# Optimization experiments

Measured on AMD Instinct MI355X. Metric: run time of the kernel, lower is better.

The kernel has to match this reference:

```python
import jax, jax.numpy as jnp
import numpy as np

HEADS = 8
EMBED = 64
FEAT_A = 256
FEAT_B = 256


def setup_inputs() -> dict:
    key = jax.random.key(0)
    k1, k2, k3, k4, k5 = jax.random.split(key, 5)
    B, N = 2, 2048
    z_a = jax.random.normal(k1, (B, FEAT_A, N), dtype=jnp.float32)
    z_b = jax.random.normal(k2, (B, FEAT_B, N), dtype=jnp.float32)
    # Conv1d(k=1, bias=False) weights, squeezed: [out_ch, in_ch]
    W_a = jax.random.normal(k3, (HEADS * EMBED, FEAT_A), dtype=jnp.float32) * (1.0 / np.sqrt(FEAT_A))
    W_b = jax.random.normal(k4, (HEADS * EMBED, FEAT_B), dtype=jnp.float32) * (1.0 / np.sqrt(FEAT_B))
    W_c = jax.random.normal(k5, (FEAT_A, HEADS * FEAT_B), dtype=jnp.float32) * (1.0 / np.sqrt(HEADS * FEAT_B))
    return {"z_a": z_a, "z_b": z_b, "W_a": W_a, "W_b": W_b, "W_c": W_c}


def reference(z_a, z_b, W_a, W_b, W_c):
    B, Fa, Na = z_a.shape
    Fb = z_b.shape[1]
    H, E = HEADS, EMBED
    norm = 1.0 / np.sqrt(E)
    # 1x1 conv embeddings -> q, k: [B, H, E, N]
    q = jnp.einsum('of,bfn->bon', W_a, z_a).reshape(B, H, E, Na)
    k = jnp.einsum('of,bfn->bon', W_b, z_b).reshape(B, H, E, -1)
    v = z_b  # [B, Fb, K]
    # coeff_pre_softmax[b,h,q,k] = (q^T k) / sqrt(E)
    pre = jnp.einsum('bheq,bhek->bhqk', q, k) * norm
    coeff = jax.nn.softmax(pre, axis=-1)  # softmax over keys (dim=2 in torch bmm form)
    # l1 loss: mean |pre| over (q,k) per head, averaged over heads
    l1 = jnp.mean(jnp.abs(pre), axis=(1, 2, 3))  # [B]
    # feat[b,h,q,f] = coeff @ v^T
    feat = jnp.einsum('bhqk,bfk->bhqf', coeff, v)
    # combine heads: w[h] = W_c[:, h*Fb:(h+1)*Fb].T  -> [H, Fb, Fa]
    w = W_c.reshape(Fa, H, Fb).transpose(1, 2, 0)
    out = jnp.einsum('bhqf,hfo->bqo', feat, w)  # sum over heads
    return out, l1
```

## Files before the change

### kernel.cpp

```cpp
#include <hip/hip_runtime.h>
#include <hip/hip_bf16.h>


#define B_ 2
#define N_ 2048
#define F_ 256
#define H_ 8
#define E_ 64

typedef __attribute__((ext_vector_type(8))) short bf16x8;
typedef __attribute__((ext_vector_type(4))) float f32x4;

__device__ __forceinline__ unsigned short f2b(float x) {
  __hip_bfloat16 h = __float2bfloat16(x);
  return *reinterpret_cast<unsigned short*>(&h);
}

__device__ __forceinline__ unsigned short f2bt(float x) {
  union { float f; unsigned u; } c; c.f = x;
  return (unsigned short)(c.u >> 16);
}

__device__ __forceinline__ f32x4 mfma16(bf16x8 a, bf16x8 b, f32x4 c) {
  return __builtin_amdgcn_mfma_f32_16x16x32_bf16(a, b, c, 0, 0, 0);
}

__device__ __forceinline__ void async_lds16(const unsigned short* g, unsigned short* l) {
  __builtin_amdgcn_global_load_lds(
      (const __attribute__((address_space(1))) unsigned int*)g,
      (__attribute__((address_space(3))) unsigned int*)l, 16, 0, 0);
}

__global__ __launch_bounds__(256) void prep_kernel(
    const float* __restrict__ W_c, unsigned short* __restrict__ wcb,
    const float* __restrict__ W_a, const float* __restrict__ W_b,
    unsigned short* __restrict__ wab, float* __restrict__ l1acc) {
  int i = blockIdx.x * 256 + threadIdx.x;
  if (i < B_) l1acc[i] = 0.f;
  const int nwc = F_ * H_ * F_ / 4;
  const int nw = 512 * F_ / 4;
  const float* src; unsigned short* dst; int j;
  if (i < nwc) { src = W_c; dst = wcb; j = i; }
  else if (i < nwc + nw) { src = W_a; dst = wab; j = i - nwc; }
  else { j = i - nwc - nw; src = W_b; dst = wab + 512 * F_; }
  float4 v = reinterpret_cast<const float4*>(src)[j];
  unsigned long long pk =
      ((unsigned long long)f2b(v.w) << 48) | ((unsigned long long)f2b(v.z) << 32) |
      ((unsigned long long)f2b(v.y) << 16) | (unsigned long long)f2b(v.x);
  reinterpret_cast<unsigned long long*>(dst)[j] = pk;
}

__global__ __launch_bounds__(256) void fused_tp(
    const float* __restrict__ z_a, const float* __restrict__ z_b,
    const unsigned short* __restrict__ wab, unsigned short* __restrict__ vbf,
    unsigned short* __restrict__ qT, unsigned short* __restrict__ kT) {
  __shared__ unsigned int t32[64][33];
  __shared__ __align__(16) unsigned short As[32][256];

  const int tid = threadIdx.x;
  const int nt = blockIdx.x, oh = blockIdx.y, wz = blockIdx.z;
  const int b = wz & 1, which = wz >> 1;
  const float* src = (which ? z_b : z_a) + (size_t)b * F_ * N_;

  const int n4 = (tid & 7) * 4;
  const int frow = tid >> 3;
  const int n_l = tid & 31;
  const int jb = tid >> 5;

#pragma unroll
  for (int s = 0; s < 4; ++s) {
#pragma unroll
    for (int pass = 0; pass < 2; ++pass) {
      int f_l = pass * 32 + frow;
      float4 v = *reinterpret_cast<const float4*>(
          &src[(size_t)(s * 64 + f_l) * N_ + nt * 32 + n4]);
      unsigned short u0 = f2b(v.x), u1 = f2b(v.y), u2 = f2b(v.z), u3 = f2b(v.w);
      t32[f_l][n4] = u0; t32[f_l][n4 + 1] = u1;
      t32[f_l][n4 + 2] = u2; t32[f_l][n4 + 3] = u3;
      if (which && oh == 0) {
        ushort4 pk = {u0, u1, u2, u3};
        *reinterpret_cast<ushort4*>(
            &vbf[(size_t)(b * F_ + s * 64 + f_l) * 2048 + nt * 32 + n4]) = pk;
      }
    }
    __syncthreads();
    {
      int c = s * 8 + jb;
      int p = c ^ n_l;
      unsigned w0 = t32[jb * 8 + 0][n_l] | (t32[jb * 8 + 1][n_l] << 16);
      unsigned w1 = t32[jb * 8 + 2][n_l] | (t32[jb * 8 + 3][n_l] << 16);
      unsigned w2 = t32[jb * 8 + 4][n_l] | (t32[jb * 8 + 5][n_l] << 16);
      unsigned w3 = t32[jb * 8 + 6][n_l] | (t32[jb * 8 + 7][n_l] << 16);
      uint4 pk = {w0, w1, w2, w3};
      *reinterpret_cast<uint4*>(&As[n_l][p * 8]) = pk;
    }
    __syncthreads();
  }

  const int wid = tid >> 6, lane = tid & 63;
  const int quad = lane >> 4, l16 = lane & 15;
  const unsigned short* wsrc = wab + (size_t)which * 512 * F_;
  unsigned short* dst = (which ? kT : qT) + (size_t)b * N_ * 512;
  const float scale = which ? 1.f : 0.125f;
  const f32x4 zero4 = {0.f, 0.f, 0.f, 0.f};

#pragma unroll
  for (int ot = 0; ot < 4; ++ot) {
    const int o = (oh * 4 + ot) * 64 + wid * 16 + l16;
    const unsigned short* brow = wsrc + (size_t)o * F_ + quad * 8;
    f32x4 acc0 = zero4, acc1 = zero4;
#pragma unroll
    for (int kt = 0; kt < 8; ++kt) {
      bf16x8 bf = *reinterpret_cast<const bf16x8*>(brow + kt * 32);
      const int row0 = l16, row1 = 16 + l16;
      bf16x8 a0 = *reinterpret_cast<const bf16x8*>(
          &As[0][0] + row0 * 256 + ((kt * 4 + quad) ^ row0) * 8);
      bf16x8 a1 = *reinterpret_cast<const bf16x8*>(
          &As[0][0] + row1 * 256 + ((kt * 4 + quad) ^ row1) * 8);
      acc0 = mfma16(a0, bf, acc0);
      acc1 = mfma16(a1, bf, acc1);
    }
#pragma unroll
    for (int r = 0; r < 4; ++r) {
      dst[(size_t)(nt * 32 + quad * 4 + r) * 512 + o] = f2b(acc0[r] * scale);
      dst[(size_t)(nt * 32 + 16 + quad * 4 + r) * 512 + o] = f2b(acc1[r] * scale);
    }
  }
}

__global__ __launch_bounds__(256, 3) void attn_mfma(
    const unsigned short* __restrict__ qT, const unsigned short* __restrict__ kT,
    const unsigned short* __restrict__ vbf, unsigned short* __restrict__ feat,
    float* __restrict__ l1acc) {
  __shared__ __align__(16) unsigned short ks[2][32][64];
  __shared__ __align__(16) unsigned short vs[2][256][32];
  __shared__ __align__(16) unsigned short p_blk[2][64][40];
  __shared__ float lsum_sh[64];
  __shared__ float redblk[256];

  const int tid = threadIdx.x;
  const int wid = tid >> 6, lane = tid & 63;
  const int quad = lane >> 4, l16 = lane & 15;
  const int qt = blockIdx.x, h = blockIdx.y, b = blockIdx.z;

  const int kkey = wid * 8 + (lane >> 3);
  const int kchunk = (lane & 7) ^ ((kkey >> 1) & 7);
  const unsigned short* kgl =
      kT + ((size_t)(b * N_ + kkey) * 512) + h * 64 + kchunk * 8;
  const unsigned short* vgl[4];
#pragma unroll
  for (int j = 0; j < 4; ++j) {
    int f = (wid * 4 + j) * 16 + (lane >> 2);
    int c = (lane & 3) ^ ((f >> 1) & 3);
    vgl[j] = vbf + ((size_t)(b * F_ + f) * 2048) + c * 8;
  }

  const unsigned short* qrow =
      qT + (size_t)(b * N_ + qt * 64 + wid * 16 + l16) * 512 + h * 64 + quad * 8;
  bf16x8 qf0 = *reinterpret_cast<const bf16x8*>(qrow);
  bf16x8 qf1 = *reinterpret_cast<const bf16x8*>(qrow + 32);

  const int koff = ((quad ^ (l16 & 7)) * 8);
  const int voff = ((quad ^ ((l16 >> 1) & 3)) * 8);

  f32x4 acc[4][4];
  const f32x4 zero4 = {0.f, 0.f, 0.f, 0.f};
#pragma unroll
  for (int g = 0; g < 4; ++g)
#pragma unroll
    for (int t = 0; t < 4; ++t) acc[g][t] = zero4;
  float lsum[4] = {0.f, 0.f, 0.f, 0.f};
  float suml1 = 0.f;
  bf16x8 vreg[4];

  async_lds16(kgl, &ks[0][wid * 8][0]);
#pragma unroll
  for (int j = 0; j < 4; ++j) async_lds16(vgl[j], &vs[0][(wid * 4 + j) * 16][0]);
  __syncthreads();

#pragma unroll 2
  for (int kt = 0; kt < N_ / 32; ++kt) {
    const int cur = kt & 1;
    if (kt + 1 < N_ / 32) {
      async_lds16(kgl + (size_t)(kt + 1) * 32 * 512, &ks[cur ^ 1][wid * 8][0]);
#pragma unroll
      for (int j = 0; j < 4; ++j)
        async_lds16(vgl[j] + (kt + 1) * 32, &vs[cur ^ 1][(wid * 4 + j) * 16][0]);
    }

    const unsigned short* ksc = &ks[cur][0][0];
    bf16x8 kf00 = *reinterpret_cast<const bf16x8*>(ksc + (2 * l16) * 64 + koff);
    bf16x8 kf01 = *reinterpret_cast<const bf16x8*>(ksc + (2 * l16) * 64 + (koff ^ 32));
    bf16x8 kf10 = *reinterpret_cast<const bf16x8*>(ksc + (2 * l16 + 1) * 64 + koff);
    bf16x8 kf11 = *reinterpret_cast<const bf16x8*>(ksc + (2 * l16 + 1) * 64 + (koff ^ 32));

    f32x4 s0 = mfma16(qf0, kf00, zero4); s0 = mfma16(qf1, kf01, s0);
    f32x4 s1 = mfma16(qf0, kf10, zero4); s1 = mfma16(qf1, kf11, s1);

#pragma unroll
    for (int r = 0; r < 4; ++r) {
      float a0 = s0[r], a1 = s1[r];
      suml1 += fabsf(a0) + fabsf(a1);
      float p0 = __expf(a0), p1 = __expf(a1);
      lsum[r] += p0 + p1;
      unsigned pk = ((unsigned)f2bt(p1) << 16) | f2bt(p0);
      *reinterpret_cast<unsigned*>(&p_blk[cur][wid * 16 + quad * 4 + r][2 * l16]) = pk;
    }

    if (kt > 0) {
#pragma unroll
      for (int g = 0; g < 4; ++g) {
        bf16x8 pf = *reinterpret_cast<const bf16x8*>(&p_blk[cur ^ 1][g * 16 + l16][quad * 8]);
#pragma unroll
        for (int t = 0; t < 4; ++t) acc[g][t] = mfma16(pf, vreg[t], acc[g][t]);
      }
    }

    {
      const unsigned short* vsc = &vs[cur][0][0];
#pragma unroll
      for (int t = 0; t < 4; ++t) {
        int f = wid * 64 + t * 16 + l16;
        vreg[t] = *reinterpret_cast<const bf16x8*>(vsc + f * 32 + voff);
      }
    }
    __syncthreads();
  }

  {
#pragma unroll
    for (int g = 0; g < 4; ++g) {
      bf16x8 pf = *reinterpret_cast<const bf16x8*>(&p_blk[1][g * 16 + l16][quad * 8]);
#pragma unroll
      for (int t = 0; t < 4; ++t) acc[g][t] = mfma16(pf, vreg[t], acc[g][t]);
    }
  }

#pragma unroll
  for (int r = 0; r < 4; ++r) {
    float rs = lsum[r];
    rs += __shfl_xor(rs, 1);
    rs += __shfl_xor(rs, 2);
    rs += __shfl_xor(rs, 4);
    rs += __shfl_xor(rs, 8);
    if (l16 == 0) lsum_sh[wid * 16 + quad * 4 + r] = rs;
  }
  __syncthreads();

#pragma unroll
  for (int g = 0; g < 4; ++g)
#pragma unroll
    for (int r = 0; r < 4; ++r) {
      float invl = 1.f / lsum_sh[g * 16 + quad * 4 + r];
      unsigned short* fr =
          feat + (size_t)(b * N_ + qt * 64 + g * 16 + quad * 4 + r) * 2048 +
          h * 256 + wid * 64 + l16;
#pragma unroll
      for (int t = 0; t < 4; ++t) fr[t * 16] = f2b(acc[g][t][r] * invl);
    }

  redblk[tid] = suml1;
  __syncthreads();
  for (int st = 128; st > 0; st >>= 1) {
    if (tid < st) redblk[tid] += redblk[tid + st];
    __syncthreads();
  }
  if (tid == 0) atomicAdd(&l1acc[b], redblk[0]);
}

__global__ __launch_bounds__(256) void combine_mfma(
    const unsigned short* __restrict__ feat, const unsigned short* __restrict__ wcb,
    const float* __restrict__ l1acc, float* __restrict__ out) {
  __shared__ __align__(16) unsigned short As[2][32][256];

  const int tid = threadIdx.x;
  const int wid = tid >> 6, lane = tid & 63;
  const int quad = lane >> 4, l16 = lane & 15;
  const int mb = blockIdx.x, ob = blockIdx.y;

  const int srow_hi = lane >> 5;
  const int spos = lane & 31;

  const unsigned short* brow = wcb + (size_t)(ob * 64 + wid * 16 + l16) * 2048 + quad * 8;

  f32x4 acc[2];
  const f32x4 zero4 = {0.f, 0.f, 0.f, 0.f};
  acc[0] = zero4; acc[1] = zero4;

#pragma unroll
  for (int i = 0; i < 4; ++i) {
    int row = wid * 8 + 2 * i + srow_hi;
    int cg = spos ^ row;
    async_lds16(feat + (size_t)(mb * 32 + row) * 2048 + cg * 8,
                &As[0][wid * 8 + 2 * i][0]);
  }
  __syncthreads();

  for (int ch = 0; ch < 8; ++ch) {
    const int cur = ch & 1;
    if (ch + 1 < 8) {
#pragma unroll
      for (int i = 0; i < 4; ++i) {
        int row = wid * 8 + 2 * i + srow_hi;
        int cg = spos ^ row;
        async_lds16(feat + (size_t)(mb * 32 + row) * 2048 + (ch + 1) * 256 + cg * 8,
                    &As[cur ^ 1][wid * 8 + 2 * i][0]);
      }
    }
#pragma unroll
    for (int kt = 0; kt < 8; ++kt) {
      bf16x8 bf = *reinterpret_cast<const bf16x8*>(brow + ch * 256 + kt * 32);
#pragma unroll
      for (int g = 0; g < 2; ++g) {
        int row = g * 16 + l16;
        int p = (kt * 4 + quad) ^ row;
        bf16x8 af = *reinterpret_cast<const bf16x8*>(&As[cur][0][0] + row * 256 + p * 8);
        acc[g] = mfma16(af, bf, acc[g]);
      }
    }
    __syncthreads();
  }

#pragma unroll
  for (int g = 0; g < 2; ++g)
#pragma unroll
    for (int r = 0; r < 4; ++r)
      out[(size_t)(mb * 32 + g * 16 + quad * 4 + r) * 256 + ob * 64 + wid * 16 + l16] =
          acc[g][r];

  if (mb == 0 && ob == 0 && tid < B_)
    out[(size_t)B_ * N_ * F_ + tid] = l1acc[tid] * (1.f / (float)(H_ * N_ * N_));
}

extern "C" void kernel_launch(void* const* d_in, const int* in_sizes, int n_in,
                              void* d_out, int out_size, void* d_ws, size_t ws_size,
                              hipStream_t stream) {
  const float* z_a = (const float*)d_in[0];
  const float* z_b = (const float*)d_in[1];
  const float* W_a = (const float*)d_in[2];
  const float* W_b = (const float*)d_in[3];
  const float* W_c = (const float*)d_in[4];
  float* out = (float*)d_out;

  char* ws = (char*)d_ws;
  unsigned short* qT = (unsigned short*)ws;
  unsigned short* kT = (unsigned short*)(ws + ((size_t)4 << 20));
  unsigned short* vbf = (unsigned short*)(ws + ((size_t)8 << 20));
  unsigned short* wcb = (unsigned short*)(ws + ((size_t)10 << 20));
  unsigned short* wab = (unsigned short*)(ws + ((size_t)15 << 20));
  float* l1acc = (float*)(ws + ((size_t)15 << 20) + (768 << 10));
  unsigned short* feat = (unsigned short*)(ws + ((size_t)16 << 20));

  const int nprep = F_ * H_ * F_ / 4 + 2 * (512 * F_ / 4);
  prep_kernel<<<dim3(nprep / 256), 256, 0, stream>>>(
      W_c, wcb, W_a, W_b, wab, l1acc);
  fused_tp<<<dim3(N_ / 32, 2, 4), 256, 0, stream>>>(z_a, z_b, wab, vbf, qT, kT);
  attn_mfma<<<dim3(N_ / 64, H_, B_), 256, 0, stream>>>(qT, kT, vbf, feat, l1acc);
  combine_mfma<<<dim3(B_ * N_ / 32, 4), 256, 0, stream>>>(feat, wcb, l1acc, out);
}
```

Baseline: 163.1 us.

## Keep softmax probabilities in registers via cross-lane shuffles instead of LDS

Computes the score tile transposed (K as the A operand) so that each wave's probabilities can be rearranged into the PV MFMA B-operand with lane shuffles. This removes the shared-memory p_blk round trip and the one-iteration software pipelining of the PV product. Each wave now owns 16 query rows across all 256 features instead of 64 rows by 64 features, which enables vectorized ushort4 stores and a shuffle-only row-sum reduction. The cost is more V fragment loads from LDS per wave (16 per step instead of 4) and 8 shuffles per iteration.

```diff
diff --git a/kernel.cpp b/kernel.cpp
--- a/kernel.cpp
+++ b/kernel.cpp
@@ -134,8 +134,6 @@
     float* __restrict__ l1acc) {
   __shared__ __align__(16) unsigned short ks[2][32][64];
   __shared__ __align__(16) unsigned short vs[2][256][32];
-  __shared__ __align__(16) unsigned short p_blk[2][64][40];
-  __shared__ float lsum_sh[64];
   __shared__ float redblk[256];
 
   const int tid = threadIdx.x;
@@ -160,23 +158,24 @@
   bf16x8 qf0 = *reinterpret_cast<const bf16x8*>(qrow);
   bf16x8 qf1 = *reinterpret_cast<const bf16x8*>(qrow + 32);
 
-  const int koff = ((quad ^ (l16 & 7)) * 8);
+  const int koff2 = ((quad ^ ((l16 >> 1) & 7)) * 8);
   const int voff = ((quad ^ ((l16 >> 1) & 3)) * 8);
 
-  f32x4 acc[4][4];
+  f32x4 acc[16];
   const f32x4 zero4 = {0.f, 0.f, 0.f, 0.f};
 #pragma unroll
-  for (int g = 0; g < 4; ++g)
-#pragma unroll
-    for (int t = 0; t < 4; ++t) acc[g][t] = zero4;
-  float lsum[4] = {0.f, 0.f, 0.f, 0.f};
+  for (int ft = 0; ft < 16; ++ft) acc[ft] = zero4;
+  float lsum_p = 0.f;
   float suml1 = 0.f;
-  bf16x8 vreg[4];
 
   async_lds16(kgl, &ks[0][wid * 8][0]);
 #pragma unroll
   for (int j = 0; j < 4; ++j) async_lds16(vgl[j], &vs[0][(wid * 4 + j) * 16][0]);
   __syncthreads();
+
+  const int srcLo = l16 + ((quad & 1) << 5);
+  const int srcHi = srcLo + 16;
+  const bool hiB = (quad >= 2);
 
 #pragma unroll 2
   for (int kt = 0; kt < N_ / 32; ++kt) {
@@ -189,75 +188,69 @@
     }
 
     const unsigned short* ksc = &ks[cur][0][0];
-    bf16x8 kf00 = *reinterpret_cast<const bf16x8*>(ksc + (2 * l16) * 64 + koff);
-    bf16x8 kf01 = *reinterpret_cast<const bf16x8*>(ksc + (2 * l16) * 64 + (koff ^ 32));
-    bf16x8 kf10 = *reinterpret_cast<const bf16x8*>(ksc + (2 * l16 + 1) * 64 + koff);
-    bf16x8 kf11 = *reinterpret_cast<const bf16x8*>(ksc + (2 * l16 + 1) * 64 + (koff ^ 32));
-
-    f32x4 s0 = mfma16(qf0, kf00, zero4); s0 = mfma16(qf1, kf01, s0);
-    f32x4 s1 = mfma16(qf0, kf10, zero4); s1 = mfma16(qf1, kf11, s1);
-
+    bf16x8 ka0 = *reinterpret_cast<const bf16x8*>(ksc + l16 * 64 + koff2);
+    bf16x8 ka1 = *reinterpret_cast<const bf16x8*>(ksc + l16 * 64 + (koff2 ^ 32));
+    bf16x8 kb0 = *reinterpret_cast<const bf16x8*>(ksc + (16 + l16) * 64 + koff2);
+    bf16x8 kb1 = *reinterpret_cast<const bf16x8*>(ksc + (16 + l16) * 64 + (koff2 ^ 32));
+
+    f32x4 d1 = mfma16(ka0, qf0, zero4); d1 = mfma16(ka1, qf1, d1);
+    f32x4 d2 = mfma16(kb0, qf0, zero4); d2 = mfma16(kb1, qf1, d2);
+
+    float p1[4], p2[4];
 #pragma unroll
     for (int r = 0; r < 4; ++r) {
-      float a0 = s0[r], a1 = s1[r];
+      float a0 = d1[r], a1 = d2[r];
       suml1 += fabsf(a0) + fabsf(a1);
-      float p0 = __expf(a0), p1 = __expf(a1);
-      lsum[r] += p0 + p1;
-      unsigned pk = ((unsigned)f2bt(p1) << 16) | f2bt(p0);
-      *reinterpret_cast<unsigned*>(&p_blk[cur][wid * 16 + quad * 4 + r][2 * l16]) = pk;
-    }
-
-    if (kt > 0) {
-#pragma unroll
-      for (int g = 0; g < 4; ++g) {
-        bf16x8 pf = *reinterpret_cast<const bf16x8*>(&p_blk[cur ^ 1][g * 16 + l16][quad * 8]);
-#pragma unroll
-        for (int t = 0; t < 4; ++t) acc[g][t] = mfma16(pf, vreg[t], acc[g][t]);
-      }
-    }
-
-    {
-      const unsigned short* vsc = &vs[cur][0][0];
-#pragma unroll
-      for (int t = 0; t < 4; ++t) {
-        int f = wid * 64 + t * 16 + l16;
-        vreg[t] = *reinterpret_cast<const bf16x8*>(vsc + f * 32 + voff);
-      }
-    }
-    __syncthreads();
-  }
+      p1[r] = __expf(a0); p2[r] = __expf(a1);
+      lsum_p += p1[r] + p2[r];
+    }
+    unsigned a01 = (unsigned)f2bt(p1[0]) | ((unsigned)f2bt(p1[1]) << 16);
+    unsigned a23 = (unsigned)f2bt(p1[2]) | ((unsigned)f2bt(p1[3]) << 16);
+    unsigned b01 = (unsigned)f2bt(p2[0]) | ((unsigned)f2bt(p2[1]) << 16);
+    unsigned b23 = (unsigned)f2bt(p2[2]) | ((unsigned)f2bt(p2[3]) << 16);
+
+    unsigned sa0 = (unsigned)__shfl((int)a01, srcLo);
+    unsigned sa1 = (unsigned)__shfl((int)a23, srcLo);
+    unsigned sa2 = (unsigned)__shfl((int)a01, srcHi);
+    unsigned sa3 = (unsigned)__shfl((int)a23, srcHi);
+    unsigned sb0 = (unsigned)__shfl((int)b01, srcLo);
+    unsigned sb1 = (unsigned)__shfl((int)b23, srcLo);
+    unsigned sb2 = (unsigned)__shfl((int)b01, srcHi);
+    unsigned sb3 = (unsigned)__shfl((int)b23, srcHi);
+    union { unsigned u[4]; bf16x8 v; } pu;
+    pu.u[0] = hiB ? sb0 : sa0;
+    pu.u[1] = hiB ? sb1 : sa1;
+    pu.u[2] = hiB ? sb2 : sa2;
+    pu.u[3] = hiB ? sb3 : sa3;
+    bf16x8 pfrag = pu.v;
+
+    const unsigned short* vsc = &vs[cur][0][0];
+#pragma unroll
+    for (int ft = 0; ft < 16; ++ft) {
+      bf16x8 vf = *reinterpret_cast<const bf16x8*>(
+          vsc + (ft * 16 + l16) * 32 + voff);
+      acc[ft] = mfma16(vf, pfrag, acc[ft]);
+    }
+
+    __syncthreads();
+  }
+
+  float rs = lsum_p;
+  rs += __shfl_xor(rs, 16);
+  rs += __shfl_xor(rs, 32);
+  float invl = 1.f / rs;
 
   {
-#pragma unroll
-    for (int g = 0; g < 4; ++g) {
-      bf16x8 pf = *reinterpret_cast<const bf16x8*>(&p_blk[1][g * 16 + l16][quad * 8]);
-#pragma unroll
-      for (int t = 0; t < 4; ++t) acc[g][t] = mfma16(pf, vreg[t], acc[g][t]);
-    }
-  }
-
-#pragma unroll
-  for (int r = 0; r < 4; ++r) {
-    float rs = lsum[r];
-    rs += __shfl_xor(rs, 1);
-    rs += __shfl_xor(rs, 2);
-    rs += __shfl_xor(rs, 4);
-    rs += __shfl_xor(rs, 8);
-    if (l16 == 0) lsum_sh[wid * 16 + quad * 4 + r] = rs;
-  }
-  __syncthreads();
-
-#pragma unroll
-  for (int g = 0; g < 4; ++g)
-#pragma unroll
-    for (int r = 0; r < 4; ++r) {
-      float invl = 1.f / lsum_sh[g * 16 + quad * 4 + r];
-      unsigned short* fr =
-          feat + (size_t)(b * N_ + qt * 64 + g * 16 + quad * 4 + r) * 2048 +
-          h * 256 + wid * 64 + l16;
-#pragma unroll
-      for (int t = 0; t < 4; ++t) fr[t * 16] = f2b(acc[g][t][r] * invl);
-    }
+    unsigned short* fr =
+        feat + (size_t)(b * N_ + qt * 64 + wid * 16 + l16) * 2048 +
+        h * 256 + quad * 4;
+#pragma unroll
+    for (int ft = 0; ft < 16; ++ft) {
+      ushort4 pk = {f2b(acc[ft][0] * invl), f2b(acc[ft][1] * invl),
+                    f2b(acc[ft][2] * invl), f2b(acc[ft][3] * invl)};
+      *reinterpret_cast<ushort4*>(fr + ft * 16) = pk;
+    }
+  }
 
   redblk[tid] = suml1;
   __syncthreads();
```

After: 170.4 us. 4.5% more time.
